# Optimization experiments

Hardware: AMD Instinct MI355X
Metric: run time of the kernel (lower is better)

## Reference

```python
import jax, jax.numpy as jnp
import numpy as np

D_MODEL = 768
NUM_HEADS = 12
DEPTH = D_MODEL // NUM_HEADS


def setup_inputs() -> dict:
    key = jax.random.key(0)
    ks = jax.random.split(key, 11)
    B, S, D = 2, 2048, D_MODEL
    scale = 1.0 / np.sqrt(D)
    inp = {
        "v": jax.random.normal(ks[0], (B, S, D), jnp.float32),
        "k": jax.random.normal(ks[1], (B, S, D), jnp.float32),
        "q": jax.random.normal(ks[2], (B, S, D), jnp.float32),
        "wq": jax.random.normal(ks[3], (D, D), jnp.float32) * scale,
        "bq": jnp.zeros((D,), jnp.float32),
        "wk": jax.random.normal(ks[4], (D, D), jnp.float32) * scale,
        "bk": jnp.zeros((D,), jnp.float32),
        "wv": jax.random.normal(ks[5], (D, D), jnp.float32) * scale,
        "bv": jnp.zeros((D,), jnp.float32),
        "wo": jax.random.normal(ks[6], (D, D), jnp.float32) * scale,
        "bo": jnp.zeros((D,), jnp.float32),
    }
    return inp


def _split_heads(x):
    # (B, S, D) -> (B, H, S, depth)
    B, S, _ = x.shape
    return x.reshape(B, S, NUM_HEADS, DEPTH).transpose(0, 2, 1, 3)


def reference(v, k, q, wq, bq, wk, bk, wv, bv, wo, bo):
    B, S, D = q.shape
    qh = _split_heads(q @ wq + bq)  # (B,H,S,dh)
    kh = _split_heads(k @ wk + bk)
    vh = _split_heads(v @ wv + bv)
    logits = jnp.einsum("bhqd,bhkd->bhqk", qh, kh) / jnp.sqrt(
        jnp.asarray(DEPTH, qh.dtype)
    )
    attn = jax.nn.softmax(logits, axis=-1)  # (B,H,S,S)
    ctx = jnp.einsum("bhqk,bhkd->bhqd", attn, vh)
    ctx = ctx.transpose(0, 2, 1, 3).reshape(B, S, D)
    return ctx @ wo + bo
```

## Files before the change

kernel.cpp:

```cpp
#include <hip/hip_runtime.h>
#include <hip/hip_bf16.h>
#include <math.h>

typedef __bf16 bf16;
typedef __attribute__((ext_vector_type(8))) __bf16 bf16x8;
typedef __attribute__((ext_vector_type(4))) __bf16 bf16x4v;
typedef __attribute__((ext_vector_type(4))) float f32x4;

#define MFMA16(a, b, c) __builtin_amdgcn_mfma_f32_16x16x32_bf16(a, b, c, 0, 0, 0)

__device__ __forceinline__ void gld16(const bf16* g, bf16* l) {
  __builtin_amdgcn_global_load_lds((const __attribute__((address_space(1))) void*)g,
                                   (__attribute__((address_space(3))) void*)l, 16, 0, 0);
}

__global__ __launch_bounds__(256) void prep(const float* __restrict__ q,
                                            const float* __restrict__ k,
                                            const float* __restrict__ v,
                                            bf16* __restrict__ qb, bf16* __restrict__ kb,
                                            bf16* __restrict__ vb,
                                            const float* __restrict__ w0,
                                            const float* __restrict__ w1,
                                            const float* __restrict__ w2,
                                            const float* __restrict__ w3,
                                            bf16* __restrict__ t0, bf16* __restrict__ t1,
                                            bf16* __restrict__ t2, bf16* __restrict__ t3) {
  const int lin = blockIdx.x;
  if (lin < 4608) {
    const int which = lin / 1536, idx = lin % 1536;
    const float* a = which == 0 ? q : (which == 1 ? k : v);
    bf16* o = which == 0 ? qb : (which == 1 ? kb : vb);
    const size_t i = ((size_t)idx * 256 + threadIdx.x) * 8;
    const float4 f0 = *(const float4*)(a + i);
    const float4 f1 = *(const float4*)(a + i + 4);
    bf16x8 r = {(bf16)f0.x, (bf16)f0.y, (bf16)f0.z, (bf16)f0.w,
                (bf16)f1.x, (bf16)f1.y, (bf16)f1.z, (bf16)f1.w};
    *(bf16x8*)(o + i) = r;
  } else {
    const int w = lin - 4608;
    const int z = w / 576, rem = w % 576;
    const int by = rem / 24, bx = rem % 24;
    const float* W = z == 0 ? w0 : (z == 1 ? w1 : (z == 2 ? w2 : w3));
    bf16* T = z == 0 ? t0 : (z == 1 ? t1 : (z == 2 ? t2 : t3));
    __shared__ float t[32][33];
    const int tx = threadIdx.x & 31, ty = threadIdx.x >> 5;
    const int c0 = bx * 32, r0 = by * 32;
#pragma unroll
    for (int i = 0; i < 4; ++i) {
      const int r = ty + 8 * i;
      t[r][tx] = W[(size_t)(r0 + r) * 768 + c0 + tx];
    }
    __syncthreads();
#pragma unroll
    for (int i = 0; i < 4; ++i) {
      const int r = ty + 8 * i;
      T[(size_t)(c0 + r) * 768 + r0 + tx] = (bf16)t[tx][r];
    }
  }
}

__device__ __forceinline__ void gemm_core(const bf16* __restrict__ A, const bf16* __restrict__ BT,
                                          int row0, int col0, bf16* As, bf16* Bs,
                                          f32x4 acc[4][4]) {
  const int tid = threadIdx.x;
  const int lane = tid & 63, wave = tid >> 6;
  const int m15 = lane & 15, kg = lane >> 4;
  const int wm = wave >> 1, wn = wave & 1;
  const int pr16 = lane & 15;
  const int pk8 = (lane >> 4) * 8;
#pragma unroll
  for (int i = 0; i < 4; ++i)
#pragma unroll
    for (int j = 0; j < 4; ++j) acc[i][j] = f32x4{0.f, 0.f, 0.f, 0.f};

  for (int k0 = 0; k0 < 768; k0 += 32) {
#pragma unroll
    for (int j = 0; j < 2; ++j) {
      const int i = wave * 2 + j;
      gld16(A + (size_t)(row0 + 16 * i + pr16) * 768 + k0 + pk8, As + i * 512);
      gld16(BT + (size_t)(col0 + 16 * i + pr16) * 768 + k0 + pk8, Bs + i * 512);
    }
    __syncthreads();
    bf16x8 af[4], bfr[4];
#pragma unroll
    for (int t = 0; t < 4; ++t)
      af[t] = *(const bf16x8*)(As + (4 * wm + t) * 512 + kg * 128 + m15 * 8);
#pragma unroll
    for (int t = 0; t < 4; ++t)
      bfr[t] = *(const bf16x8*)(Bs + (4 * wn + t) * 512 + kg * 128 + m15 * 8);
#pragma unroll
    for (int mt = 0; mt < 4; ++mt)
#pragma unroll
      for (int nt = 0; nt < 4; ++nt) acc[mt][nt] = MFMA16(af[mt], bfr[nt], acc[mt][nt]);
    __syncthreads();
  }
}

__global__ __launch_bounds__(256, 3) void gemm_qkv(
    const bf16* __restrict__ qb, const bf16* __restrict__ kb, const bf16* __restrict__ vb,
    const bf16* __restrict__ wqT, const bf16* __restrict__ wkT, const bf16* __restrict__ wvT,
    const float* __restrict__ bq, const float* __restrict__ bk, const float* __restrict__ bv,
    bf16* __restrict__ Qh, bf16* __restrict__ Kh, bf16* __restrict__ Vt) {
  __shared__ bf16 As[128 * 32], Bs[128 * 32];
  const bf16 *A, *BT;
  const float* bias;
  bf16* out;
  int mode;
  if (blockIdx.z == 0) { A = qb; BT = wqT; bias = bq; out = Qh; mode = 0; }
  else if (blockIdx.z == 1) { A = kb; BT = wkT; bias = bk; out = Kh; mode = 0; }
  else { A = vb; BT = wvT; bias = bv; out = Vt; mode = 1; }
  const int row0 = blockIdx.y * 128, col0 = blockIdx.x * 128;
  f32x4 acc[4][4];
  gemm_core(A, BT, row0, col0, As, Bs, acc);

  const int lane = threadIdx.x & 63, wave = threadIdx.x >> 6;
  const int m15 = lane & 15, kg = lane >> 4;
  const int wm = wave >> 1, wn = wave & 1;
#pragma unroll
  for (int mt = 0; mt < 4; ++mt) {
#pragma unroll
    for (int nt = 0; nt < 4; ++nt) {
      const int col = col0 + 64 * wn + 16 * nt + m15;
      const float bb = bias[col];
      const int h = col >> 6, d = col & 63;
      const int rowb = row0 + 64 * wm + 16 * mt + kg * 4;
      const int b = rowb >> 11, s0 = rowb & 2047;
      if (mode == 0) {
#pragma unroll
        for (int r = 0; r < 4; ++r)
          out[((size_t)(b * 12 + h) * 2048 + s0 + r) * 64 + d] = (bf16)(acc[mt][nt][r] + bb);
      } else {
        bf16x4v pk;
#pragma unroll
        for (int r = 0; r < 4; ++r) pk[r] = (bf16)(acc[mt][nt][r] + bb);
        *(bf16x4v*)&out[((size_t)(b * 12 + h) * 64 + d) * 2048 + s0] = pk;
      }
    }
  }
}

__global__ __launch_bounds__(256, 3) void gemm_out(const bf16* __restrict__ A,
                                                   const bf16* __restrict__ BT,
                                                   const float* __restrict__ bias,
                                                   float* __restrict__ out) {
  __shared__ bf16 As[64 * 32], Bs[64 * 32];
  const int tid = threadIdx.x;
  const int lane = tid & 63, wave = tid >> 6;
  const int m15 = lane & 15, kg = lane >> 4;
  const int wm = wave >> 1, wn = wave & 1;
  const int row0 = blockIdx.y * 64, col0 = blockIdx.x * 64;
  const int pr16 = lane & 15, pk8 = (lane >> 4) * 8;

  f32x4 acc[2][2];
#pragma unroll
  for (int i = 0; i < 2; ++i)
#pragma unroll
    for (int j = 0; j < 2; ++j) acc[i][j] = f32x4{0.f, 0.f, 0.f, 0.f};

  for (int k0 = 0; k0 < 768; k0 += 32) {
    gld16(A + (size_t)(row0 + 16 * wave + pr16) * 768 + k0 + pk8, As + wave * 512);
    gld16(BT + (size_t)(col0 + 16 * wave + pr16) * 768 + k0 + pk8, Bs + wave * 512);
    __syncthreads();
    bf16x8 af[2], bfr[2];
#pragma unroll
    for (int t = 0; t < 2; ++t)
      af[t] = *(const bf16x8*)(As + (2 * wm + t) * 512 + kg * 128 + m15 * 8);
#pragma unroll
    for (int t = 0; t < 2; ++t)
      bfr[t] = *(const bf16x8*)(Bs + (2 * wn + t) * 512 + kg * 128 + m15 * 8);
#pragma unroll
    for (int mt = 0; mt < 2; ++mt)
#pragma unroll
      for (int nt = 0; nt < 2; ++nt) acc[mt][nt] = MFMA16(af[mt], bfr[nt], acc[mt][nt]);
    __syncthreads();
  }
#pragma unroll
  for (int mt = 0; mt < 2; ++mt) {
#pragma unroll
    for (int nt = 0; nt < 2; ++nt) {
      const int col = col0 + 32 * wn + 16 * nt + m15;
      const float bb = bias[col];
#pragma unroll
      for (int r = 0; r < 4; ++r) {
        const int row = row0 + 32 * wm + 16 * mt + kg * 4 + r;
        out[(size_t)row * 768 + col] = acc[mt][nt][r] + bb;
      }
    }
  }
}

__global__ __launch_bounds__(256, 3) void attn_kernel(const bf16* __restrict__ Q,
                                                      const bf16* __restrict__ K,
                                                      const bf16* __restrict__ VT,
                                                      bf16* __restrict__ ctx) {
  __shared__ __align__(16) bf16 S[21504];

  const int tid = threadIdx.x;
  const int lane = tid & 63, wave = tid >> 6;
  const int m15 = lane & 15, kg = lane >> 4;
  const int lin = blockIdx.x;
  const int bh = lin % 24, qblk = lin / 24;
  const size_t hb = (size_t)bh * 2048 * 64;
  const bf16* Qp = Q + hb;
  const bf16* Kp = K + hb;
  const bf16* Vp = VT + hb;
  const int pipe = wave >> 1;
  const int qrow0 = qblk * 64 + (wave & 1) * 32;
  bf16* Pw = S + 16384 + wave * 1280;

  const int kpr = lane & 7, kpc = (lane >> 3) * 8;
  const int vpr = lane & 15, vpc = (lane >> 4) * 8;

  bf16x8 qf[2][2];
#pragma unroll
  for (int t = 0; t < 2; ++t)
#pragma unroll
    for (int ks = 0; ks < 2; ++ks) {
      bf16x8 tv = *(const bf16x8*)&Qp[(size_t)(qrow0 + 16 * t + m15) * 64 + 32 * ks + kg * 8];
#pragma unroll
      for (int j = 0; j < 8; ++j) tv[j] = (bf16)((float)tv[j] * 0.125f);
      qf[t][ks] = tv;
    }

  f32x4 o[2][4];
  float lp[2][4];
#pragma unroll
  for (int t = 0; t < 2; ++t) {
#pragma unroll
    for (int nt = 0; nt < 4; ++nt) o[t][nt] = f32x4{0.f, 0.f, 0.f, 0.f};
#pragma unroll
    for (int r = 0; r < 4; ++r) lp[t][r] = 0.f;
  }

#pragma unroll
  for (int j = 0; j < 4; ++j) {
    const int idx = wave * 4 + j;
    const int sp = idx >> 3, r8 = idx & 7;
    const int kc = sp * 1024;
    if (r8 < 4)
      gld16(Kp + (size_t)(kc + 8 * r8 + kpr) * 64 + kpc, S + sp * 2 * 2048 + r8 * 512);
    else {
      const int i = r8 - 4;
      gld16(Vp + (size_t)(16 * i + vpr) * 2048 + kc + vpc, S + 8192 + sp * 2 * 2048 + i * 512);
    }
  }

  for (int c = 0; c < 32; ++c) {
    const int buf = c & 1;
    __syncthreads();
    if (c < 31) {
      const int nb = buf ^ 1;
#pragma unroll
      for (int j = 0; j < 4; ++j) {
        const int idx = wave * 4 + j;
        const int sp = idx >> 3, r8 = idx & 7;
        const int kc = sp * 1024 + (c + 1) * 32;
        if (r8 < 4)
          gld16(Kp + (size_t)(kc + 8 * r8 + kpr) * 64 + kpc,
                S + (sp * 2 + nb) * 2048 + r8 * 512);
        else {
          const int i = r8 - 4;
          gld16(Vp + (size_t)(16 * i + vpr) * 2048 + kc + vpc,
                S + 8192 + (sp * 2 + nb) * 2048 + i * 512);
        }
      }
    }
    const bf16* KsB = S + (pipe * 2 + buf) * 2048;
    const bf16* VsB = S + 8192 + (pipe * 2 + buf) * 2048;

    f32x4 s[2][2];
#pragma unroll
    for (int t = 0; t < 2; ++t)
#pragma unroll
      for (int nt = 0; nt < 2; ++nt) s[t][nt] = f32x4{0.f, 0.f, 0.f, 0.f};
#pragma unroll
    for (int ks = 0; ks < 2; ++ks) {
#pragma unroll
      for (int nt = 0; nt < 2; ++nt) {
        const int key = 16 * nt + m15;
        const bf16x8 kf =
            *(const bf16x8*)&KsB[(key >> 3) * 512 + (4 * ks + kg) * 64 + (key & 7) * 8];
        s[0][nt] = MFMA16(qf[0][ks], kf, s[0][nt]);
        s[1][nt] = MFMA16(qf[1][ks], kf, s[1][nt]);
      }
    }
#pragma unroll
    for (int t = 0; t < 2; ++t)
#pragma unroll
      for (int r = 0; r < 4; ++r)
#pragma unroll
        for (int nt = 0; nt < 2; ++nt) {
          const float pe = __expf(s[t][nt][r]);
          lp[t][r] += pe;
          Pw[t * 640 + (kg * 4 + r) * 40 + 16 * nt + m15] = (bf16)pe;
        }
    asm volatile("s_waitcnt lgkmcnt(0)" ::: "memory");
    const bf16x8 pf0 = *(const bf16x8*)&Pw[0 * 640 + m15 * 40 + kg * 8];
    const bf16x8 pf1 = *(const bf16x8*)&Pw[1 * 640 + m15 * 40 + kg * 8];
#pragma unroll
    for (int nt = 0; nt < 4; ++nt) {
      const int d = 16 * nt + m15;
      const bf16x8 vf =
          *(const bf16x8*)&VsB[(d >> 4) * 512 + kg * 128 + (d & 15) * 8];
      o[0][nt] = MFMA16(pf0, vf, o[0][nt]);
      o[1][nt] = MFMA16(pf1, vf, o[1][nt]);
    }
  }

  __syncthreads();
  float* sc = (float*)S;
  if (wave >= 2) {
    const int rg = (wave - 2) * 2560;
#pragma unroll
    for (int t = 0; t < 2; ++t)
#pragma unroll
      for (int nt = 0; nt < 4; ++nt)
        *(f32x4*)&sc[rg + (t * 4 + nt) * 256 + lane * 4] = o[t][nt];
    f32x4 l0 = {lp[0][0], lp[0][1], lp[0][2], lp[0][3]};
    f32x4 l1 = {lp[1][0], lp[1][1], lp[1][2], lp[1][3]};
    *(f32x4*)&sc[rg + 2048 + lane * 8] = l0;
    *(f32x4*)&sc[rg + 2048 + lane * 8 + 4] = l1;
  }
  __syncthreads();
  if (wave < 2) {
    const int rg = wave * 2560;
#pragma unroll
    for (int t = 0; t < 2; ++t)
#pragma unroll
      for (int nt = 0; nt < 4; ++nt) {
        const f32x4 po = *(const f32x4*)&sc[rg + (t * 4 + nt) * 256 + lane * 4];
#pragma unroll
        for (int j = 0; j < 4; ++j) o[t][nt][j] += po[j];
      }
    const f32x4 pl0 = *(const f32x4*)&sc[rg + 2048 + lane * 8];
    const f32x4 pl1 = *(const f32x4*)&sc[rg + 2048 + lane * 8 + 4];
#pragma unroll
    for (int r = 0; r < 4; ++r) { lp[0][r] += pl0[r]; lp[1][r] += pl1[r]; }
#pragma unroll
    for (int t = 0; t < 2; ++t)
#pragma unroll
      for (int r = 0; r < 4; ++r) {
#pragma unroll
        for (int st = 1; st < 16; st <<= 1) lp[t][r] += __shfl_xor(lp[t][r], st);
      }
    const int b = bh / 12, h = bh % 12;
#pragma unroll
    for (int t = 0; t < 2; ++t)
#pragma unroll
      for (int nt = 0; nt < 4; ++nt)
#pragma unroll
        for (int r = 0; r < 4; ++r) {
          const int sr = qrow0 + 16 * t + kg * 4 + r;
          ctx[((size_t)(b * 2048) + sr) * 768 + h * 64 + 16 * nt + m15] =
              (bf16)(o[t][nt][r] / lp[t][r]);
        }
  }
}

extern "C" void kernel_launch(void* const* d_in, const int* in_sizes, int n_in,
                              void* d_out, int out_size, void* d_ws, size_t ws_size,
                              hipStream_t stream) {
  const float* v = (const float*)d_in[0];
  const float* k = (const float*)d_in[1];
  const float* q = (const float*)d_in[2];
  const float* wq = (const float*)d_in[3];
  const float* bq = (const float*)d_in[4];
  const float* wk = (const float*)d_in[5];
  const float* bk = (const float*)d_in[6];
  const float* wv = (const float*)d_in[7];
  const float* bv = (const float*)d_in[8];
  const float* wo = (const float*)d_in[9];
  const float* bo = (const float*)d_in[10];

  char* ws = (char*)d_ws;
  const size_t SEG = (size_t)4096 * 768 * sizeof(bf16);
  const size_t WSEG = (size_t)768 * 768 * sizeof(bf16);
  bf16* Qh = (bf16*)(ws + 0 * SEG);
  bf16* Kh = (bf16*)(ws + 1 * SEG);
  bf16* Vt = (bf16*)(ws + 2 * SEG);
  bf16* qb = (bf16*)(ws + 3 * SEG);
  bf16* kb = (bf16*)(ws + 4 * SEG);
  bf16* vb = (bf16*)(ws + 5 * SEG);
  bf16* ctx = qb;
  bf16* wqT = (bf16*)(ws + 6 * SEG);
  bf16* wkT = (bf16*)(ws + 6 * SEG + WSEG);
  bf16* wvT = (bf16*)(ws + 6 * SEG + 2 * WSEG);
  bf16* woT = (bf16*)(ws + 6 * SEG + 3 * WSEG);

  prep<<<dim3(6912), 256, 0, stream>>>(q, k, v, qb, kb, vb, wq, wk, wv, wo,
                                       wqT, wkT, wvT, woT);
  gemm_qkv<<<dim3(6, 32, 3), 256, 0, stream>>>(qb, kb, vb, wqT, wkT, wvT, bq, bk, bv,
                                               Qh, Kh, Vt);
  attn_kernel<<<dim3(768), 256, 0, stream>>>(Qh, Kh, Vt, ctx);
  gemm_out<<<dim3(12, 64), 256, 0, stream>>>(ctx, woT, bo, (float*)d_out);
}
```

Before: 216.2 us.

## Give each wave private K/V buffers and drop per-iteration block barriers

Each wave now loads its own copy of the K/V tiles into a private double buffer and waits on its own vmcnt instead of a block-wide __syncthreads each iteration. Loads are issued two chunks ahead, after the current chunk's LDS reads are done. The cost is that waves sharing a pipe load the same data twice, LDS use roughly doubles, and launch bounds drop occupancy from 3 to 2 blocks per CU.

Result: slower. 254.6 us (+17.8%).

```diff
diff --git a/kernel.cpp b/kernel.cpp
--- a/kernel.cpp
+++ b/kernel.cpp
@@ -189,11 +189,11 @@
   }
 }
 
-__global__ __launch_bounds__(256, 3) void attn_kernel(const bf16* __restrict__ Q,
+__global__ __launch_bounds__(256, 2) void attn_kernel(const bf16* __restrict__ Q,
                                                       const bf16* __restrict__ K,
                                                       const bf16* __restrict__ VT,
                                                       bf16* __restrict__ ctx) {
-  __shared__ __align__(16) bf16 S[21504];
+  __shared__ __align__(16) bf16 S[37888];
 
   const int tid = threadIdx.x;
   const int lane = tid & 63, wave = tid >> 6;
@@ -206,7 +206,10 @@
   const bf16* Vp = VT + hb;
   const int pipe = wave >> 1;
   const int qrow0 = qblk * 64 + (wave & 1) * 32;
-  bf16* Pw = S + 16384 + wave * 1280;
+
+  bf16* Kw = S + wave * 4096;
+  bf16* Vw = S + 16384 + wave * 4096;
+  bf16* Pw = S + 32768 + wave * 1280;
 
   const int kpr = lane & 7, kpc = (lane >> 3) * 8;
   const int vpr = lane & 15, vpc = (lane >> 4) * 8;
@@ -232,41 +235,30 @@
     for (int r = 0; r < 4; ++r) lp[t][r] = 0.f;
   }
 
-#pragma unroll
-  for (int j = 0; j < 4; ++j) {
-    const int idx = wave * 4 + j;
-    const int sp = idx >> 3, r8 = idx & 7;
-    const int kc = sp * 1024;
-    if (r8 < 4)
-      gld16(Kp + (size_t)(kc + 8 * r8 + kpr) * 64 + kpc, S + sp * 2 * 2048 + r8 * 512);
-    else {
-      const int i = r8 - 4;
-      gld16(Vp + (size_t)(16 * i + vpr) * 2048 + kc + vpc, S + 8192 + sp * 2 * 2048 + i * 512);
-    }
-  }
+  auto stage = [&](int cc, int b) {
+    const int kc = pipe * 1024 + cc * 32;
+#pragma unroll
+    for (int j = 0; j < 4; ++j)
+      gld16(Kp + (size_t)(kc + 8 * j + kpr) * 64 + kpc, Kw + b * 2048 + j * 512);
+#pragma unroll
+    for (int i = 0; i < 4; ++i)
+      gld16(Vp + (size_t)(16 * i + vpr) * 2048 + kc + vpc, Vw + b * 2048 + i * 512);
+  };
+
+  stage(0, 0);
+  stage(1, 1);
 
   for (int c = 0; c < 32; ++c) {
     const int buf = c & 1;
-    __syncthreads();
     if (c < 31) {
-      const int nb = buf ^ 1;
-#pragma unroll
-      for (int j = 0; j < 4; ++j) {
-        const int idx = wave * 4 + j;
-        const int sp = idx >> 3, r8 = idx & 7;
-        const int kc = sp * 1024 + (c + 1) * 32;
-        if (r8 < 4)
-          gld16(Kp + (size_t)(kc + 8 * r8 + kpr) * 64 + kpc,
-                S + (sp * 2 + nb) * 2048 + r8 * 512);
-        else {
-          const int i = r8 - 4;
-          gld16(Vp + (size_t)(16 * i + vpr) * 2048 + kc + vpc,
-                S + 8192 + (sp * 2 + nb) * 2048 + i * 512);
-        }
-      }
-    }
-    const bf16* KsB = S + (pipe * 2 + buf) * 2048;
-    const bf16* VsB = S + 8192 + (pipe * 2 + buf) * 2048;
+      asm volatile("s_waitcnt vmcnt(8)" ::: "memory");
+    } else {
+      asm volatile("s_waitcnt vmcnt(0)" ::: "memory");
+    }
+    __builtin_amdgcn_sched_barrier(0);
+
+    const bf16* KsB = Kw + buf * 2048;
+    const bf16* VsB = Vw + buf * 2048;
 
     f32x4 s[2][2];
 #pragma unroll
@@ -295,6 +287,7 @@
           Pw[t * 640 + (kg * 4 + r) * 40 + 16 * nt + m15] = (bf16)pe;
         }
     asm volatile("s_waitcnt lgkmcnt(0)" ::: "memory");
+    __builtin_amdgcn_sched_barrier(0);
     const bf16x8 pf0 = *(const bf16x8*)&Pw[0 * 640 + m15 * 40 + kg * 8];
     const bf16x8 pf1 = *(const bf16x8*)&Pw[1 * 640 + m15 * 40 + kg * 8];
 #pragma unroll
@@ -304,6 +297,11 @@
           *(const bf16x8*)&VsB[(d >> 4) * 512 + kg * 128 + (d & 15) * 8];
       o[0][nt] = MFMA16(pf0, vf, o[0][nt]);
       o[1][nt] = MFMA16(pf1, vf, o[1][nt]);
+    }
+    if (c < 30) {
+      asm volatile("s_waitcnt lgkmcnt(0)" ::: "memory");
+      __builtin_amdgcn_sched_barrier(0);
+      stage(c + 2, buf);
     }
   }
 
```
